# Performance work log

Hardware: AMD Instinct MI355X
Metric: run time of the kernel (lower is better)

## Reference

```python
import jax, jax.numpy as jnp
import numpy as np

WS = [2048, 4096, 8192]
RS = [1, 2, 4]
OFFSET = 0
NEG = -1e30


def _causal_attn(xseg, Wq, Wk, Wv, Wo):
    """xseg: (b, s, m, c). Returns (out (b,s,m,c), denom (b,s,m)) where denom is
    the softmax denominator sum_j exp(score_ij) per query (computed stably via lse)."""
    c = xseg.shape[-1]
    m = xseg.shape[-2]
    q = jnp.einsum('bsmc,cd->bsmd', xseg, Wq)
    k = jnp.einsum('bsmc,cd->bsmd', xseg, Wk)
    v = jnp.einsum('bsmc,cd->bsmd', xseg, Wv)
    scores = jnp.einsum('bsid,bsjd->bsij', q, k) / jnp.sqrt(jnp.asarray(c, xseg.dtype))
    causal = jnp.tril(jnp.ones((m, m), dtype=bool))
    scores = jnp.where(causal, scores, NEG)
    lse = jax.nn.logsumexp(scores, axis=-1)            # (b,s,m)
    p = jnp.exp(scores - lse[..., None])               # softmax
    o = jnp.einsum('bsij,bsjd->bsid', p, v)
    o = jnp.einsum('bsid,dc->bsic', o, Wo)
    return o, jnp.exp(lse)


def setup_inputs() -> dict:
    key = jax.random.key(0)
    kx, kq, kk, kv, ko = jax.random.split(key, 5)
    b, n, c = 4, 8192, 128
    scale = 1.0 / np.sqrt(c)  # keep activations O(1) so exp(lse) stays finite
    return {
        'x': jax.random.normal(kx, (b, n, c), dtype=jnp.float32),
        'Wq': jax.random.normal(kq, (c, c), dtype=jnp.float32) * scale,
        'Wk': jax.random.normal(kk, (c, c), dtype=jnp.float32) * scale,
        'Wv': jax.random.normal(kv, (c, c), dtype=jnp.float32) * scale,
        'Wo': jax.random.normal(ko, (c, c), dtype=jnp.float32) * scale,
    }


def reference(x, Wq, Wk, Wv, Wo):
    b, n, c = x.shape
    denom_sums = jnp.zeros((b, n), dtype=x.dtype)
    branches = []
    for w, r in zip(WS, RS):
        s = n // w
        # gather dilated tokens within each segment: (b, s, m, c)
        xr = x.reshape(b, s, w, c)[:, :, OFFSET::r, :]
        m = xr.shape[2]
        o, d = _causal_attn(xr, Wq, Wk, Wv, Wo)
        # global positions of the gathered tokens, flattened over (segment, within-seg)
        idx = (jnp.arange(s)[:, None] * w + OFFSET + r * jnp.arange(m)[None, :]).reshape(-1)
        d_flat = d.reshape(b, s * m)
        o_flat = o.reshape(b, s * m, c)
        denom_sums = denom_sums.at[:, idx].add(d_flat)
        branches.append((idx, o_flat, d_flat))
    out = jnp.zeros_like(x)
    for idx, o_flat, d_flat in branches:
        alpha = d_flat / denom_sums[:, idx]             # (b, s*m)
        out = out.at[:, idx].add(o_flat * alpha[..., None])
    return out
```

## Files before the change

### kernel.cpp

```cpp
#include <hip/hip_runtime.h>
#include <hip/hip_bf16.h>

typedef __attribute__((ext_vector_type(8))) __bf16 bf16x8;
typedef __attribute__((ext_vector_type(4))) float f32x4;
typedef __attribute__((ext_vector_type(8))) unsigned short u16x8;

#define DEVI __device__ __forceinline__
#define MFMA(a,b,c) __builtin_amdgcn_mfma_f32_16x16x32_bf16((a),(b),(c),0,0,0)
#define EXP2F(x) __builtin_exp2f(x)
#define LOG2F(x) __builtin_log2f(x)

DEVI unsigned short f2bf(float f){ __bf16 h = (__bf16)f; return __builtin_bit_cast(unsigned short, h); }
DEVI float bf2f(unsigned short u){ unsigned int x = ((unsigned int)u) << 16; return __builtin_bit_cast(float, x); }
DEVI bf16x8 ld_bf8(const void* p){ u16x8 u = *(const u16x8*)p; return __builtin_bit_cast(bf16x8, u); }
DEVI f32x4 splat4(float x){ f32x4 v = {x,x,x,x}; return v; }
DEVI f32x4 vmax4(f32x4 a, f32x4 b){
  f32x4 r;
  #pragma unroll
  for (int i=0;i<4;++i) r[i]=fmaxf(a[i],b[i]);
  return r;
}
DEVI void gload_lds16(const void* g, void* l){
  void* g2 = const_cast<void*>(g);
  __builtin_amdgcn_global_load_lds((__attribute__((address_space(1))) void*)g2,
                                   (__attribute__((address_space(3))) void*)l, 16, 0, 0);
}

__device__ const unsigned int SCHED[30] = {
  0x100C000Bu, 0x110C0C0Bu, 0x050C0005u, 0x1C0B0A0Fu, 0x1D0B150Fu,
  0x0E0B000Au, 0x0F0B0B0Au, 0x1B0A000Fu, 0x180A000Eu, 0x190A0A0Eu,
  0x1A0A140Eu, 0x170A120Du, 0x0C0A0009u, 0x0D0A0A09u, 0x040A0004u,
  0x1509000Du, 0x1609090Du, 0x1309080Cu, 0x1409110Cu, 0x0A090008u,
  0x0B090908u, 0x1208000Cu, 0x08080007u, 0x09080807u, 0x03080003u,
  0x06070006u, 0x07070706u, 0x02060002u, 0x01040001u, 0x00020000u
};
__device__ const int CB[16] = {0,1,2,3,4,5,6,8,10,12,14,16,18,21,24,27};

__global__ __launch_bounds__(256) void k_prep(const float* __restrict__ Wq, const float* __restrict__ Wk,
                                              const float* __restrict__ Wv, const float* __restrict__ Wo,
                                              unsigned short* __restrict__ wT){
  int i = blockIdx.x*256 + threadIdx.x;
  int mat = i >> 14, col = (i >> 7) & 127, k = i & 127;
  const float* W = (mat==0)?Wq:(mat==1)?Wk:(mat==2)?Wv:Wo;
  float v = W[k*128 + col];
  if (mat == 0) v *= 0.12754245006257017f;
  wT[i] = f2bf(v);
}

__global__ __launch_bounds__(256) void k_qkv(const float* __restrict__ x, const unsigned short* __restrict__ wT,
                                             unsigned short* __restrict__ Qo, unsigned short* __restrict__ Ko,
                                             unsigned short* __restrict__ VT0, unsigned short* __restrict__ VT1,
                                             unsigned short* __restrict__ VT2){
  __shared__ unsigned short Tl[128*130];
  const int tid=threadIdx.x, lane=tid&63, wid=tid>>6, ll=lane&15, hi=lane>>4;
  const int row0g = blockIdx.x*128;
  const long row0 = (long)row0g + wid*32;
  bf16x8 a[2][4];
  #pragma unroll
  for (int mt=0;mt<2;++mt){
    const float* xr = x + (row0 + mt*16 + ll)*128 + hi*8;
    #pragma unroll
    for (int ks=0;ks<4;++ks){
      f32x4 f0 = *(const f32x4*)(const void*)(xr + ks*32);
      f32x4 f1 = *(const f32x4*)(const void*)(xr + ks*32 + 4);
      u16x8 u;
      #pragma unroll
      for (int j=0;j<4;++j){ u[j]=f2bf(f0[j]); u[j+4]=f2bf(f1[j]); }
      a[mt][ks] = __builtin_bit_cast(bf16x8, u);
    }
  }
  #pragma unroll
  for (int m3=0;m3<3;++m3){
    const unsigned short* wp = wT + m3*16384 + ll*128 + hi*8;
    #pragma unroll
    for (int nt=0;nt<8;++nt){
      f32x4 acc0=splat4(0.f), acc1=splat4(0.f);
      #pragma unroll
      for (int ks=0;ks<4;++ks){
        bf16x8 b = ld_bf8(wp + nt*2048 + ks*32);
        acc0 = MFMA(a[0][ks], b, acc0);
        acc1 = MFMA(a[1][ks], b, acc1);
      }
      if (m3 < 2){
        unsigned short* outp = (m3==0)?Qo:Ko;
        #pragma unroll
        for (int r=0;r<4;++r){
          outp[(row0 + hi*4 + r)*128 + nt*16 + ll]      = f2bf(acc0[r]);
          outp[(row0 + 16 + hi*4 + r)*128 + nt*16 + ll] = f2bf(acc1[r]);
        }
      } else {
        #pragma unroll
        for (int r=0;r<4;++r){
          Tl[(wid*32 + hi*4 + r)*130 + nt*16 + ll]      = f2bf(acc0[r]);
          Tl[(wid*32 + 16 + hi*4 + r)*130 + nt*16 + ll] = f2bf(acc1[r]);
        }
      }
    }
  }
  __syncthreads();
  int tk = 2*lane;
  int pp0 = (tk>>5)*32 + ((tk>>4)&1)*4 + ((tk&15)>>2)*8 + (tk&3);
  #pragma unroll 4
  for (int p=0;p<32;++p){
    int d = wid*32 + p;
    unsigned int w0 = (unsigned int)Tl[(2*lane)*130 + d] | ((unsigned int)Tl[(2*lane+1)*130 + d] << 16);
    *(unsigned int*)(VT0 + (long)d*32768 + row0g + pp0) = w0;
    if (lane < 32){
      unsigned int w1 = (unsigned int)Tl[(4*lane)*130 + d] | ((unsigned int)Tl[(4*lane+2)*130 + d] << 16);
      *(unsigned int*)(VT1 + (long)d*16384 + (row0g>>1) + pp0) = w1;
    }
    if (lane < 16){
      unsigned int w2 = (unsigned int)Tl[(8*lane)*130 + d] | ((unsigned int)Tl[(8*lane+4)*130 + d] << 16);
      *(unsigned int*)(VT2 + (long)d*8192 + (row0g>>2) + pp0) = w2;
    }
  }
}

__global__ __launch_bounds__(256,3) void k_attn(
    const unsigned short* __restrict__ Qg, const unsigned short* __restrict__ Kg,
    const unsigned short* __restrict__ VT0, const unsigned short* __restrict__ VT1,
    const unsigned short* __restrict__ VT2,
    unsigned short* __restrict__ OP, float* __restrict__ LP){
  __shared__ unsigned char smem[49152];

  const int tid=threadIdx.x, lane=tid&63, wid=tid>>6, ll=lane&15, hi=lane>>4;

  int x = blockIdx.x & 7;
  int i = blockIdx.x >> 3;
  int sid, r;
  if (i < 60){
    r = i >> 2; int k = i & 3;
    if (k < 3){ sid = 3*x + k; }
    else { sid = 24 + (x >> 1); if (x & 1) r += 15; }
  } else {
    int t = i - 60; r = 15 + t/3; sid = 3*x + t%3;
  }
  unsigned int e = SCHED[r];
  int qb   = (int)(e & 255u);
  int t032 = (int)((e >> 8) & 255u) * 2;
  int n32  = (int)((e >> 16) & 255u) * 2;
  int slot = (int)(e >> 24);
  int br, bb, seg;
  if (sid < 16){ br=0; bb=sid>>2; seg=sid&3; }
  else if (sid < 24){ br=1; bb=(sid-16)>>1; seg=(sid-16)&1; }
  else { br=2; bb=sid-24; seg=0; }
  const int rstr = 1 << br;
  const long g0 = (long)bb*8192 + (long)seg*(2048 << br);
  const int P = sid*30 + slot;
  const unsigned short* VTb = (br==0)?VT0:(br==1)?VT1:VT2;
  const int NC = 32768 >> br;
  const int rb0 = (int)(g0 >> br);

  const int qrow_w = qb*128 + wid*32;

  bf16x8 aq[2][4];
  #pragma unroll
  for (int mt=0;mt<2;++mt){
    long gq = g0 + (long)rstr*(qrow_w + mt*16 + ll);
    const unsigned short* qp = Qg + gq*128 + hi*8;
    #pragma unroll
    for (int ks=0;ks<4;++ks) aq[mt][ks] = ld_bf8(qp + ks*32);
  }

  f32x4 o[2][8];
  #pragma unroll
  for (int mt=0;mt<2;++mt){
    #pragma unroll
    for (int dt=0;dt<8;++dt) o[mt][dt]=splat4(0.f);
  }
  float mrun[2], lrun[2];
  mrun[0]=mrun[1]=-1e30f; lrun[0]=lrun[1]=0.f;

#define STAGE(ktv, bslot)                                                              \
  {                                                                                    \
    unsigned char* Kb = smem + (bslot)*8192;                                           \
    unsigned char* Vb = smem + 24576 + (bslot)*8192;                                   \
    _Pragma("unroll")                                                                  \
    for (int i_=0;i_<2;++i_){                                                          \
      int rbase = wid*8 + i_*4;                                                        \
      int row = rbase + hi;                                                            \
      long gk = g0 + (long)rstr*((ktv)*32 + row);                                      \
      const unsigned short* src = Kg + gk*128 + ((ll ^ (row & 7)) * 8);                \
      gload_lds16((const void*)src, (void*)(Kb + rbase*256));                          \
    }                                                                                  \
    int rank_base = rb0 + (ktv)*32;                                                    \
    _Pragma("unroll")                                                                  \
    for (int i_=0;i_<2;++i_){                                                          \
      int li = i_*256 + tid;                                                           \
      int d_  = li >> 2;                                                               \
      int s_  = li & 3;                                                                \
      int g_  = (s_ - (d_>>1)) & 3;                                                    \
      const unsigned short* src = VTb + (long)d_*NC + rank_base + g_*8;                \
      gload_lds16((const void*)src, (void*)(Vb + i_*4096 + wid*1024));                 \
    }                                                                                  \
  }

  STAGE(t032, 0);
  STAGE(t032 + 1, 1);

  for (int it=0; it<n32; ++it){
    const int kt = t032 + it;
    if (it + 1 < n32){
      asm volatile("s_waitcnt vmcnt(4) lgkmcnt(0)" ::: "memory");
    } else {
      asm volatile("s_waitcnt vmcnt(0) lgkmcnt(0)" ::: "memory");
    }
    __builtin_amdgcn_s_barrier();
    __builtin_amdgcn_sched_barrier(0);

    if (it + 2 < n32){
      STAGE(kt + 2, (it + 2) % 3);
    }

    if (kt*32 <= qrow_w + 31){
      unsigned char* Kc = smem + (it % 3)*8192;
      unsigned char* Vc = smem + 24576 + (it % 3)*8192;
      f32x4 s[2][2];
      #pragma unroll
      for (int mt=0;mt<2;++mt){
        #pragma unroll
        for (int nt=0;nt<2;++nt) s[mt][nt]=splat4(0.f);
      }
      __builtin_amdgcn_s_setprio(1);
      #pragma unroll
      for (int nt=0;nt<2;++nt){
        int krow = nt*16 + ll;
        #pragma unroll
        for (int ks=0;ks<4;++ks){
          int chunk = (ks*4 + hi) ^ (krow & 7);
          bf16x8 bk = ld_bf8(Kc + krow*256 + chunk*16);
          s[0][nt] = MFMA(bk, aq[0][ks], s[0][nt]);
          s[1][nt] = MFMA(bk, aq[1][ks], s[1][nt]);
        }
      }
      __builtin_amdgcn_s_setprio(0);
      if (kt*32 + 31 > qrow_w){
        #pragma unroll
        for (int mt=0;mt<2;++mt){
          int qrow = qrow_w + mt*16 + ll;
          #pragma unroll
          for (int nt=0;nt<2;++nt){
            int kvcol = kt*32 + nt*16 + hi*4;
            #pragma unroll
            for (int rr=0;rr<4;++rr) if (kvcol + rr > qrow) s[mt][nt][rr] = -1e30f;
          }
        }
      }
      #pragma unroll
      for (int mt=0;mt<2;++mt){
        f32x4 t4 = vmax4(s[mt][0], s[mt][1]);
        float mloc = fmaxf(fmaxf(t4[0],t4[1]), fmaxf(t4[2],t4[3]));
        mloc = fmaxf(mloc, __shfl_xor(mloc, 16, 64));
        mloc = fmaxf(mloc, __shfl_xor(mloc, 32, 64));
        bool upd = __any(mloc > mrun[mt] + 8.0f);
        if (upd){
          float mnew = fmaxf(mrun[mt], mloc);
          float sc = EXP2F(mrun[mt] - mnew);
          mrun[mt] = mnew;
          lrun[mt] *= sc;
          f32x4 scv;
          #pragma unroll
          for (int rr=0;rr<4;++rr) scv[rr] = __shfl(sc, hi*4 + rr, 64);
          #pragma unroll
          for (int dt=0;dt<8;++dt) o[mt][dt] = o[mt][dt]*scv;
        }
        f32x4 tsum = splat4(0.f);
        #pragma unroll
        for (int nt=0;nt<2;++nt){
          #pragma unroll
          for (int rr=0;rr<4;++rr) s[mt][nt][rr] = EXP2F(s[mt][nt][rr] - mrun[mt]);
          tsum += s[mt][nt];
        }
        lrun[mt] += (tsum[0]+tsum[1]) + (tsum[2]+tsum[3]);
      }
      bf16x8 pa[2];
      #pragma unroll
      for (int mt=0;mt<2;++mt){
        u16x8 up;
        #pragma unroll
        for (int rr=0;rr<4;++rr){
          up[rr]   = f2bf(s[mt][0][rr]);
          up[4+rr] = f2bf(s[mt][1][rr]);
        }
        pa[mt] = __builtin_bit_cast(bf16x8, up);
      }
      __builtin_amdgcn_s_setprio(1);
      #pragma unroll
      for (int dt=0;dt<8;++dt){
        int d = dt*16 + ll;
        int sw = (hi + (d>>1)) & 3;
        bf16x8 bv = ld_bf8(Vc + d*64 + sw*16);
        o[0][dt] = MFMA(pa[0], bv, o[0][dt]);
        o[1][dt] = MFMA(pa[1], bv, o[1][dt]);
      }
      __builtin_amdgcn_s_setprio(0);
    }
  }
#undef STAGE

  unsigned short* op = OP + (long)P*16384;
  float* lp = LP + (long)P*128;
  #pragma unroll
  for (int mt=0;mt<2;++mt){
    float l = lrun[mt];
    l += __shfl_xor(l, 16, 64);
    l += __shfl_xor(l, 32, 64);
    float invs = 1.f / l;
    f32x4 iv;
    #pragma unroll
    for (int rr=0;rr<4;++rr) iv[rr] = __shfl(invs, hi*4 + rr, 64);
    #pragma unroll
    for (int dt=0;dt<8;++dt){
      f32x4 res = o[mt][dt]*iv;
      #pragma unroll
      for (int rr=0;rr<4;++rr){
        int qloc = wid*32 + mt*16 + hi*4 + rr;
        op[qloc*128 + dt*16 + ll] = f2bf(res[rr]);
      }
    }
    float lse = mrun[mt] + LOG2F(l);
    if (lane < 16){
      lp[wid*32 + mt*16 + lane] = lse;
    }
  }
}

__global__ __launch_bounds__(256) void k_comb(
    const unsigned short* __restrict__ OP, const float* __restrict__ LP,
    const unsigned short* __restrict__ wT, float* __restrict__ out){
  const int tid=threadIdx.x, lane=tid&63, wid=tid>>6, ll=lane&15, hi=lane>>4;
  const long row0 = (long)blockIdx.x*128 + wid*32;
  bf16x8 a[2][4];
  #pragma unroll
  for (int mt=0;mt<2;++mt){
    int g = (int)(row0 + mt*16 + ll);
    int bb = g >> 13;
    int posn = g & 8191;
    bool bv[3]; int pbase[3]; int ql[3]; int bn[3];
    {
      int sid = bb*4 + (posn >> 11);
      int qrow = posn & 2047;
      int qb = qrow >> 7;
      bv[0]=true; ql[0]=qrow & 127; bn[0]=(qb<6)?1:(qb<12)?2:3; pbase[0]=sid*30 + CB[qb];
    }
    if ((posn & 1) == 0){
      int p1 = posn >> 1;
      int sid = 16 + bb*2 + (p1 >> 11);
      int qrow = p1 & 2047;
      int qb = qrow >> 7;
      bv[1]=true; ql[1]=qrow & 127; bn[1]=(qb<6)?1:(qb<12)?2:3; pbase[1]=sid*30 + CB[qb];
    } else { bv[1]=false; ql[1]=0; bn[1]=0; pbase[1]=0; }
    if ((posn & 3) == 0){
      int p2 = posn >> 2;
      int sid = 24 + bb;
      int qb = p2 >> 7;
      bv[2]=true; ql[2]=p2 & 127; bn[2]=(qb<6)?1:(qb<12)?2:3; pbase[2]=sid*30 + CB[qb];
    } else { bv[2]=false; ql[2]=0; bn[2]=0; pbase[2]=0; }

    float Lx[3][3];
    #pragma unroll
    for (int b=0;b<3;++b){
      #pragma unroll
      for (int c=0;c<3;++c){
        bool v = bv[b] && (c < bn[b]);
        Lx[b][c] = v ? LP[(pbase[b]+c)*128 + ql[b]] : -1e30f;
      }
    }
    float mx = -1e30f;
    #pragma unroll
    for (int b=0;b<3;++b){
      #pragma unroll
      for (int c=0;c<3;++c) mx = fmaxf(mx, Lx[b][c]);
    }
    float W[3][3]; float wsum = 0.f;
    #pragma unroll
    for (int b=0;b<3;++b){
      #pragma unroll
      for (int c=0;c<3;++c){
        bool v = bv[b] && (c < bn[b]);
        W[b][c] = v ? EXP2F(Lx[b][c] - mx) : 0.f;
        wsum += W[b][c];
      }
    }
    float inv = 1.f / wsum;

    float y[4][8];
    #pragma unroll
    for (int ks=0;ks<4;++ks){
      #pragma unroll
      for (int jj=0;jj<8;++jj) y[ks][jj]=0.f;
    }
    #pragma unroll
    for (int b=0;b<3;++b){
      #pragma unroll
      for (int c=0;c<3;++c){
        if (bv[b] && (c < bn[b])){
          const unsigned short* p = OP + (long)(pbase[b]+c)*16384 + ql[b]*128 + hi*8;
          float wgt = W[b][c];
          #pragma unroll
          for (int ks=0;ks<4;++ks){
            u16x8 u = *(const u16x8*)(const void*)(p + ks*32);
            #pragma unroll
            for (int jj=0;jj<8;++jj) y[ks][jj] += wgt * bf2f(u[jj]);
          }
        }
      }
    }
    #pragma unroll
    for (int ks=0;ks<4;++ks){
      u16x8 u;
      #pragma unroll
      for (int jj=0;jj<8;++jj) u[jj] = f2bf(y[ks][jj]*inv);
      a[mt][ks] = __builtin_bit_cast(bf16x8, u);
    }
  }
  const unsigned short* wp = wT + 3*16384 + ll*128 + hi*8;
  #pragma unroll
  for (int nt=0;nt<8;++nt){
    f32x4 acc0=splat4(0.f), acc1=splat4(0.f);
    #pragma unroll
    for (int ks=0;ks<4;++ks){
      bf16x8 b = ld_bf8(wp + nt*2048 + ks*32);
      acc0 = MFMA(a[0][ks], b, acc0);
      acc1 = MFMA(a[1][ks], b, acc1);
    }
    #pragma unroll
    for (int rr=0;rr<4;++rr){
      out[(row0 + hi*4 + rr)*128 + nt*16 + ll] = acc0[rr];
      out[(row0 + 16 + hi*4 + rr)*128 + nt*16 + ll] = acc1[rr];
    }
  }
}

extern "C" void kernel_launch(void* const* d_in, const int* in_sizes, int n_in,
                              void* d_out, int out_size, void* d_ws, size_t ws_size,
                              hipStream_t stream){
  const float* x  = (const float*)d_in[0];
  const float* Wq = (const float*)d_in[1];
  const float* Wk = (const float*)d_in[2];
  const float* Wv = (const float*)d_in[3];
  const float* Wo = (const float*)d_in[4];
  char* ws = (char*)d_ws;
  unsigned short* wT  = (unsigned short*)(ws);
  unsigned short* Q   = (unsigned short*)(ws + 131072);
  unsigned short* K   = (unsigned short*)(ws + 8519680);
  unsigned short* VT0 = (unsigned short*)(ws + 16908288);
  unsigned short* VT1 = (unsigned short*)(ws + 25296896);
  unsigned short* VT2 = (unsigned short*)(ws + 29491200);
  unsigned short* OP  = (unsigned short*)(ws + 31588352);
  float* LP           = (float*)(ws + 59113472);
  k_prep<<<256, 256, 0, stream>>>(Wq, Wk, Wv, Wo, wT);
  k_qkv <<<256, 256, 0, stream>>>(x, wT, Q, K, VT0, VT1, VT2);
  k_attn<<<840, 256, 0, stream>>>(Q, K, VT0, VT1, VT2, OP, LP);
  k_comb<<<256, 256, 0, stream>>>(OP, LP, wT, (float*)d_out);
}
```

Baseline: 113.3 us.

## Split attention blocks into single-wave blocks loading K/V directly into registers

The attention kernel now launches one 64-thread wave per block (four times as many blocks) instead of four waves sharing LDS-staged K/V tiles. Each wave loads its K and V fragments straight from global memory into registers, prefetching the next tile, and stops its loop at its own causal bound instead of idling through tiles it does not need. This removes the LDS staging, the block barriers and causal-skip imbalance between waves. In exchange, K/V data is no longer shared across the four query waves, so global/L2 traffic rises and latency hiding depends on the register prefetch.

```diff
diff --git a/kernel.cpp b/kernel.cpp
--- a/kernel.cpp
+++ b/kernel.cpp
@@ -19,11 +19,6 @@
   #pragma unroll
   for (int i=0;i<4;++i) r[i]=fmaxf(a[i],b[i]);
   return r;
-}
-DEVI void gload_lds16(const void* g, void* l){
-  void* g2 = const_cast<void*>(g);
-  __builtin_amdgcn_global_load_lds((__attribute__((address_space(1))) void*)g2,
-                                   (__attribute__((address_space(3))) void*)l, 16, 0, 0);
 }
 
 __device__ const unsigned int SCHED[30] = {
@@ -116,17 +111,17 @@
   }
 }
 
-__global__ __launch_bounds__(256,3) void k_attn(
+__global__ __launch_bounds__(64,2) void k_attn(
     const unsigned short* __restrict__ Qg, const unsigned short* __restrict__ Kg,
     const unsigned short* __restrict__ VT0, const unsigned short* __restrict__ VT1,
     const unsigned short* __restrict__ VT2,
     unsigned short* __restrict__ OP, float* __restrict__ LP){
-  __shared__ unsigned char smem[49152];
-
-  const int tid=threadIdx.x, lane=tid&63, wid=tid>>6, ll=lane&15, hi=lane>>4;
+  const int lane=threadIdx.x&63, ll=lane&15, hi=lane>>4;
 
   int x = blockIdx.x & 7;
-  int i = blockIdx.x >> 3;
+  int ii = blockIdx.x >> 3;
+  int wid = ii & 3;
+  int i = ii >> 2;
   int sid, r;
   if (i < 60){
     r = i >> 2; int k = i & 3;
@@ -152,6 +147,8 @@
   const int rb0 = (int)(g0 >> br);
 
   const int qrow_w = qb*128 + wid*32;
+  int nloc = (qrow_w >> 5) - t032 + 1;
+  if (nloc > n32) nloc = n32;
 
   bf16x8 aq[2][4];
   #pragma unroll
@@ -171,132 +168,106 @@
   float mrun[2], lrun[2];
   mrun[0]=mrun[1]=-1e30f; lrun[0]=lrun[1]=0.f;
 
-#define STAGE(ktv, bslot)                                                              \
-  {                                                                                    \
-    unsigned char* Kb = smem + (bslot)*8192;                                           \
-    unsigned char* Vb = smem + 24576 + (bslot)*8192;                                   \
-    _Pragma("unroll")                                                                  \
-    for (int i_=0;i_<2;++i_){                                                          \
-      int rbase = wid*8 + i_*4;                                                        \
-      int row = rbase + hi;                                                            \
-      long gk = g0 + (long)rstr*((ktv)*32 + row);                                      \
-      const unsigned short* src = Kg + gk*128 + ((ll ^ (row & 7)) * 8);                \
-      gload_lds16((const void*)src, (void*)(Kb + rbase*256));                          \
-    }                                                                                  \
-    int rank_base = rb0 + (ktv)*32;                                                    \
-    _Pragma("unroll")                                                                  \
-    for (int i_=0;i_<2;++i_){                                                          \
-      int li = i_*256 + tid;                                                           \
-      int d_  = li >> 2;                                                               \
-      int s_  = li & 3;                                                                \
-      int g_  = (s_ - (d_>>1)) & 3;                                                    \
-      const unsigned short* src = VTb + (long)d_*NC + rank_base + g_*8;                \
-      gload_lds16((const void*)src, (void*)(Vb + i_*4096 + wid*1024));                 \
-    }                                                                                  \
-  }
-
-  STAGE(t032, 0);
-  STAGE(t032 + 1, 1);
-
-  for (int it=0; it<n32; ++it){
+  const unsigned short* kp0 = Kg + (g0 + (long)rstr*((long)t032*32 + ll))*128 + hi*8;
+  const unsigned short* kp1 = Kg + (g0 + (long)rstr*((long)t032*32 + 16 + ll))*128 + hi*8;
+  const long kadv = (long)rstr*32*128;
+  const unsigned short* vpb[8];
+  #pragma unroll
+  for (int dt=0;dt<8;++dt) vpb[dt] = VTb + (long)(dt*16+ll)*NC + rb0 + t032*32 + hi*8;
+
+  bf16x8 kb[2][4], vb[8];
+  #pragma unroll
+  for (int ks=0;ks<4;++ks){ kb[0][ks] = ld_bf8(kp0 + ks*32); kb[1][ks] = ld_bf8(kp1 + ks*32); }
+  #pragma unroll
+  for (int dt=0;dt<8;++dt) vb[dt] = ld_bf8(vpb[dt]);
+  kp0 += kadv; kp1 += kadv;
+
+  for (int it=0; it<nloc; ++it){
     const int kt = t032 + it;
-    if (it + 1 < n32){
-      asm volatile("s_waitcnt vmcnt(4) lgkmcnt(0)" ::: "memory");
-    } else {
-      asm volatile("s_waitcnt vmcnt(0) lgkmcnt(0)" ::: "memory");
-    }
-    __builtin_amdgcn_s_barrier();
-    __builtin_amdgcn_sched_barrier(0);
-
-    if (it + 2 < n32){
-      STAGE(kt + 2, (it + 2) % 3);
-    }
-
-    if (kt*32 <= qrow_w + 31){
-      unsigned char* Kc = smem + (it % 3)*8192;
-      unsigned char* Vc = smem + 24576 + (it % 3)*8192;
-      f32x4 s[2][2];
+    f32x4 s[2][2];
+    #pragma unroll
+    for (int mt=0;mt<2;++mt){
+      #pragma unroll
+      for (int nt=0;nt<2;++nt) s[mt][nt]=splat4(0.f);
+    }
+    __builtin_amdgcn_s_setprio(1);
+    #pragma unroll
+    for (int nt=0;nt<2;++nt){
+      #pragma unroll
+      for (int ks=0;ks<4;++ks){
+        s[0][nt] = MFMA(kb[nt][ks], aq[0][ks], s[0][nt]);
+        s[1][nt] = MFMA(kb[nt][ks], aq[1][ks], s[1][nt]);
+      }
+    }
+    __builtin_amdgcn_s_setprio(0);
+    if (it + 1 < nloc){
+      #pragma unroll
+      for (int ks=0;ks<4;++ks){ kb[0][ks] = ld_bf8(kp0 + ks*32); kb[1][ks] = ld_bf8(kp1 + ks*32); }
+      kp0 += kadv; kp1 += kadv;
+    }
+    if (kt*32 + 31 > qrow_w){
       #pragma unroll
       for (int mt=0;mt<2;++mt){
-        #pragma unroll
-        for (int nt=0;nt<2;++nt) s[mt][nt]=splat4(0.f);
-      }
-      __builtin_amdgcn_s_setprio(1);
+        int qrow = qrow_w + mt*16 + ll;
+        #pragma unroll
+        for (int nt=0;nt<2;++nt){
+          int kvcol = kt*32 + nt*16 + hi*4;
+          #pragma unroll
+          for (int rr=0;rr<4;++rr) if (kvcol + rr > qrow) s[mt][nt][rr] = -1e30f;
+        }
+      }
+    }
+    #pragma unroll
+    for (int mt=0;mt<2;++mt){
+      f32x4 t4 = vmax4(s[mt][0], s[mt][1]);
+      float mloc = fmaxf(fmaxf(t4[0],t4[1]), fmaxf(t4[2],t4[3]));
+      mloc = fmaxf(mloc, __shfl_xor(mloc, 16, 64));
+      mloc = fmaxf(mloc, __shfl_xor(mloc, 32, 64));
+      bool upd = __any(mloc > mrun[mt] + 8.0f);
+      if (upd){
+        float mnew = fmaxf(mrun[mt], mloc);
+        float sc = EXP2F(mrun[mt] - mnew);
+        mrun[mt] = mnew;
+        lrun[mt] *= sc;
+        f32x4 scv;
+        #pragma unroll
+        for (int rr=0;rr<4;++rr) scv[rr] = __shfl(sc, hi*4 + rr, 64);
+        #pragma unroll
+        for (int dt=0;dt<8;++dt) o[mt][dt] = o[mt][dt]*scv;
+      }
+      f32x4 tsum = splat4(0.f);
       #pragma unroll
       for (int nt=0;nt<2;++nt){
-        int krow = nt*16 + ll;
-        #pragma unroll
-        for (int ks=0;ks<4;++ks){
-          int chunk = (ks*4 + hi) ^ (krow & 7);
-          bf16x8 bk = ld_bf8(Kc + krow*256 + chunk*16);
-          s[0][nt] = MFMA(bk, aq[0][ks], s[0][nt]);
-          s[1][nt] = MFMA(bk, aq[1][ks], s[1][nt]);
-        }
-      }
-      __builtin_amdgcn_s_setprio(0);
-      if (kt*32 + 31 > qrow_w){
-        #pragma unroll
-        for (int mt=0;mt<2;++mt){
-          int qrow = qrow_w + mt*16 + ll;
-          #pragma unroll
-          for (int nt=0;nt<2;++nt){
-            int kvcol = kt*32 + nt*16 + hi*4;
-            #pragma unroll
-            for (int rr=0;rr<4;++rr) if (kvcol + rr > qrow) s[mt][nt][rr] = -1e30f;
-          }
-        }
-      }
-      #pragma unroll
-      for (int mt=0;mt<2;++mt){
-        f32x4 t4 = vmax4(s[mt][0], s[mt][1]);
-        float mloc = fmaxf(fmaxf(t4[0],t4[1]), fmaxf(t4[2],t4[3]));
-        mloc = fmaxf(mloc, __shfl_xor(mloc, 16, 64));
-        mloc = fmaxf(mloc, __shfl_xor(mloc, 32, 64));
-        bool upd = __any(mloc > mrun[mt] + 8.0f);
-        if (upd){
-          float mnew = fmaxf(mrun[mt], mloc);
-          float sc = EXP2F(mrun[mt] - mnew);
-          mrun[mt] = mnew;
-          lrun[mt] *= sc;
-          f32x4 scv;
-          #pragma unroll
-          for (int rr=0;rr<4;++rr) scv[rr] = __shfl(sc, hi*4 + rr, 64);
-          #pragma unroll
-          for (int dt=0;dt<8;++dt) o[mt][dt] = o[mt][dt]*scv;
-        }
-        f32x4 tsum = splat4(0.f);
-        #pragma unroll
-        for (int nt=0;nt<2;++nt){
-          #pragma unroll
-          for (int rr=0;rr<4;++rr) s[mt][nt][rr] = EXP2F(s[mt][nt][rr] - mrun[mt]);
-          tsum += s[mt][nt];
-        }
-        lrun[mt] += (tsum[0]+tsum[1]) + (tsum[2]+tsum[3]);
-      }
-      bf16x8 pa[2];
-      #pragma unroll
-      for (int mt=0;mt<2;++mt){
-        u16x8 up;
-        #pragma unroll
-        for (int rr=0;rr<4;++rr){
-          up[rr]   = f2bf(s[mt][0][rr]);
-          up[4+rr] = f2bf(s[mt][1][rr]);
-        }
-        pa[mt] = __builtin_bit_cast(bf16x8, up);
-      }
-      __builtin_amdgcn_s_setprio(1);
-      #pragma unroll
-      for (int dt=0;dt<8;++dt){
-        int d = dt*16 + ll;
-        int sw = (hi + (d>>1)) & 3;
-        bf16x8 bv = ld_bf8(Vc + d*64 + sw*16);
-        o[0][dt] = MFMA(pa[0], bv, o[0][dt]);
-        o[1][dt] = MFMA(pa[1], bv, o[1][dt]);
-      }
-      __builtin_amdgcn_s_setprio(0);
-    }
-  }
-#undef STAGE
+        #pragma unroll
+        for (int rr=0;rr<4;++rr) s[mt][nt][rr] = EXP2F(s[mt][nt][rr] - mrun[mt]);
+        tsum += s[mt][nt];
+      }
+      lrun[mt] += (tsum[0]+tsum[1]) + (tsum[2]+tsum[3]);
+    }
+    bf16x8 pa[2];
+    #pragma unroll
+    for (int mt=0;mt<2;++mt){
+      u16x8 up;
+      #pragma unroll
+      for (int rr=0;rr<4;++rr){
+        up[rr]   = f2bf(s[mt][0][rr]);
+        up[4+rr] = f2bf(s[mt][1][rr]);
+      }
+      pa[mt] = __builtin_bit_cast(bf16x8, up);
+    }
+    __builtin_amdgcn_s_setprio(1);
+    #pragma unroll
+    for (int dt=0;dt<8;++dt){
+      o[0][dt] = MFMA(pa[0], vb[dt], o[0][dt]);
+      o[1][dt] = MFMA(pa[1], vb[dt], o[1][dt]);
+    }
+    __builtin_amdgcn_s_setprio(0);
+    if (it + 1 < nloc){
+      int ro = (it + 1)*32;
+      #pragma unroll
+      for (int dt=0;dt<8;++dt) vb[dt] = ld_bf8(vpb[dt] + ro);
+    }
+  }
 
   unsigned short* op = OP + (long)P*16384;
   float* lp = LP + (long)P*128;
@@ -451,6 +422,6 @@
   float* LP           = (float*)(ws + 59113472);
   k_prep<<<256, 256, 0, stream>>>(Wq, Wk, Wv, Wo, wT);
   k_qkv <<<256, 256, 0, stream>>>(x, wT, Q, K, VT0, VT1, VT2);
-  k_attn<<<840, 256, 0, stream>>>(Q, K, VT0, VT1, VT2, OP, LP);
+  k_attn<<<3360, 64, 0, stream>>>(Q, K, VT0, VT1, VT2, OP, LP);
   k_comb<<<256, 256, 0, stream>>>(OP, LP, wT, (float*)d_out);
 }
```

New measurement: 186.0 us. 64.2% more time.
